# Kernel tuning notes

Hardware: AMD Instinct MI355X
Metric: run time of the kernel (lower is better)

## Reference

```python
import jax, jax.numpy as jnp
import numpy as np
import math

D_MODEL = 2048
N_HEADS = 16
D_HEAD = D_MODEL // N_HEADS
SCALE = 1.0 / math.sqrt(D_HEAD)


def setup_inputs() -> dict:
    key = jax.random.key(0)
    kx, kq, kk, kv, ko = jax.random.split(key, 5)
    x = jax.random.normal(kx, (2, 2048, D_MODEL), dtype=jnp.float32)
    W_q = jax.random.normal(kq, (D_MODEL, D_MODEL), dtype=jnp.float32)
    W_k = jax.random.normal(kk, (D_MODEL, D_MODEL), dtype=jnp.float32)
    W_v = jax.random.normal(kv, (D_MODEL, D_MODEL), dtype=jnp.float32) * math.sqrt(2.0 / D_MODEL)
    W_o = jax.random.normal(ko, (D_MODEL, D_MODEL), dtype=jnp.float32) * math.sqrt(2.0 / D_MODEL)
    return {"x": x, "W_q": W_q, "W_k": W_k, "W_v": W_v, "W_o": W_o}


def reference(x, W_q, W_k, W_v, W_o) -> jnp.ndarray:
    B, S, D = x.shape
    q = (x @ W_q).reshape(B, S, N_HEADS, D_HEAD)  # [b, q, h, dh]
    k = (x @ W_k).reshape(B, S, N_HEADS, D_HEAD)  # [b, k, h, dh]
    v = x @ W_v                                    # [b, k, d_model] (NOT split into heads)
    scores = jnp.einsum('bqhd,bkhd->bhqk', q, k)   # [b, h, q, k]
    # Faithful quirk: additive -1e9 causal mask applied BEFORE the scale.
    mask = jnp.triu(jnp.full((S, S), -1e9, dtype=scores.dtype), k=1)
    scores = (scores + mask) * SCALE
    probs = jax.nn.softmax(scores, axis=-1)
    # Faithful quirk: sums over heads h AND keys k against full-width v.
    out = jnp.einsum('bhqk,bkd->bqd', probs, v)    # [b, q, d_model]
    return out @ W_o
```

## Files before the change

kernel.cpp:

```cpp
#include <hip/hip_runtime.h>

typedef unsigned short u16;
typedef __attribute__((ext_vector_type(8))) short bf16x8;
typedef __attribute__((ext_vector_type(4))) float f32x4;

#define DEV __device__ __forceinline__
#define EXP2(x) __builtin_amdgcn_exp2f(x)
#define LOG2(x) __builtin_amdgcn_logf(x)

DEV u16 f2bf(float f) {
  union { float f; unsigned u; } v; v.f = f;
  unsigned r = v.u + 0x7fffu + ((v.u >> 16) & 1u);
  return (u16)(r >> 16);
}
DEV float bf2f(u16 h) {
  union { unsigned u; float f; } v; v.u = ((unsigned)h) << 16;
  return v.f;
}
DEV f32x4 mfma16(bf16x8 a, bf16x8 b, f32x4 c) {
  return __builtin_amdgcn_mfma_f32_16x16x32_bf16(a, b, c, 0, 0, 0);
}
DEV void cp16(const u16* g, u16* l) {
  __builtin_amdgcn_global_load_lds((__attribute__((address_space(1))) void*)g,
                                   (__attribute__((address_space(3))) void*)l, 16, 0, 0);
}

__global__ __launch_bounds__(256) void split_pair(const float4* __restrict__ x,
                                                  u16* __restrict__ hi, u16* __restrict__ lo) {
  const size_t i = (size_t)blockIdx.x * 256 + threadIdx.x;
  const float4 v = x[i];
  ushort4 h, l;
  h.x = f2bf(v.x); l.x = f2bf(v.x - bf2f(h.x));
  h.y = f2bf(v.y); l.y = f2bf(v.y - bf2f(h.y));
  h.z = f2bf(v.z); l.z = f2bf(v.z - bf2f(h.z));
  h.w = f2bf(v.w); l.w = f2bf(v.w - bf2f(h.w));
  *(ushort4*)&hi[i * 4] = h;
  *(ushort4*)&lo[i * 4] = l;
}

template<bool LO>
__global__ __launch_bounds__(256) void transpose_split(const float* __restrict__ W,
                                                       u16* __restrict__ Th, u16* __restrict__ Tl) {
  __shared__ float t[64][65];
  const int r0 = blockIdx.y * 64, c0 = blockIdx.x * 64;
  const int rr = threadIdx.x >> 4, c4 = (threadIdx.x & 15) * 4;
#pragma unroll
  for (int p = 0; p < 4; ++p) {
    const float4 v = *(const float4*)&W[(size_t)(r0 + p * 16 + rr) * 2048 + c0 + c4];
    t[p * 16 + rr][c4 + 0] = v.x; t[p * 16 + rr][c4 + 1] = v.y;
    t[p * 16 + rr][c4 + 2] = v.z; t[p * 16 + rr][c4 + 3] = v.w;
  }
  __syncthreads();
#pragma unroll
  for (int p = 0; p < 4; ++p) {
    const int cc = p * 16 + rr;
    const float v0 = t[c4 + 0][cc], v1 = t[c4 + 1][cc], v2 = t[c4 + 2][cc], v3 = t[c4 + 3][cc];
    ushort4 h;
    h.x = f2bf(v0); h.y = f2bf(v1); h.z = f2bf(v2); h.w = f2bf(v3);
    *(ushort4*)&Th[(size_t)(c0 + cc) * 2048 + r0 + c4] = h;
    if constexpr (LO) {
      ushort4 l;
      l.x = f2bf(v0 - bf2f(h.x)); l.y = f2bf(v1 - bf2f(h.y));
      l.z = f2bf(v2 - bf2f(h.z)); l.w = f2bf(v3 - bf2f(h.w));
      *(ushort4*)&Tl[(size_t)(c0 + cc) * 2048 + r0 + c4] = l;
    }
  }
}

template<bool SPLIT3, int OUTMODE, bool KLIM>
__global__ __launch_bounds__(256, 2) void gemm_bt(
    const u16* __restrict__ Aph, const u16* __restrict__ Apl,
    const u16* __restrict__ Bph, const u16* __restrict__ Bpl,
    const u16* __restrict__ Bph2, const u16* __restrict__ Bpl2,
    void* __restrict__ C0, void* __restrict__ C1,
    void* __restrict__ C0b, void* __restrict__ C1b,
    const int M, const int N, const int K, const int bShift) {
  extern __shared__ u16 lds[];
  constexpr int T_AL = 4096;
  constexpr int T_BH = SPLIT3 ? 8192 : 4096;
  constexpr int T_BL = 12288;
  if (blockIdx.z) { Bph = Bph2; Bpl = Bpl2; C0 = C0b; C1 = C1b; }
  const int tid = threadIdx.x;
  const int wave = tid >> 6, lane = tid & 63;
  const int li = lane & 15, l4 = lane >> 4;
  const int lin0 = ((int)blockIdx.y << 4) | (int)blockIdx.x;
  const int xcd = lin0 & 7, idx = lin0 >> 3;
  const int m0 = ((xcd << 2) | (idx & 3)) * 128;
  const int n0 = (idx >> 2) * 128;
  const int wr = (wave >> 1) * 64, wc = (wave & 1) * 64;
  const u16* Bh = Bph; const u16* Bl = Bpl;
  if (bShift) { const size_t s = (size_t)(m0 >> 11) * (size_t)bShift; Bh += s; if (SPLIT3) Bl += s; }

  const f32x4 fz = {0.f, 0.f, 0.f, 0.f};
  f32x4 acc[4][4];
#pragma unroll
  for (int m = 0; m < 4; ++m)
#pragma unroll
    for (int n = 0; n < 4; ++n) acc[m][n] = fz;

  const size_t aoff = (size_t)(m0 + (tid >> 2)) * K + (tid & 3) * 8;
  const size_t boff = (size_t)(n0 + (tid >> 2)) * K + (tid & 3) * 8;
  const size_t rstep = (size_t)64 * K;
  const int s0 = tid * 8, s1 = 2048 + tid * 8;
  const int abase = (wr + li) * 32 + l4 * 8;
  const int bbase = (wc + li) * 32 + l4 * 8;
  const int kEnd = KLIM ? ((m0 & 2047) + 128 < K ? (m0 & 2047) + 128 : K) : K;

#pragma unroll 1
  for (int k0 = 0; k0 < kEnd; k0 += 32) {
    cp16(Aph + aoff + k0,         &lds[s0]);
    cp16(Aph + aoff + rstep + k0, &lds[s1]);
    cp16(Bh + boff + k0,          &lds[T_BH + s0]);
    cp16(Bh + boff + rstep + k0,  &lds[T_BH + s1]);
    if constexpr (SPLIT3) {
      cp16(Apl + aoff + k0,         &lds[T_AL + s0]);
      cp16(Apl + aoff + rstep + k0, &lds[T_AL + s1]);
      cp16(Bl + boff + k0,          &lds[T_BL + s0]);
      cp16(Bl + boff + rstep + k0,  &lds[T_BL + s1]);
    }
    __syncthreads();
    bf16x8 af[4], bf_[4];
#pragma unroll
    for (int m = 0; m < 4; ++m) af[m] = *(const bf16x8*)&lds[abase + m * 512];
#pragma unroll
    for (int n = 0; n < 4; ++n) bf_[n] = *(const bf16x8*)&lds[T_BH + bbase + n * 512];
    if constexpr (SPLIT3) {
      bf16x8 alf[4], blf[4];
#pragma unroll
      for (int m = 0; m < 4; ++m) alf[m] = *(const bf16x8*)&lds[T_AL + abase + m * 512];
#pragma unroll
      for (int n = 0; n < 4; ++n) blf[n] = *(const bf16x8*)&lds[T_BL + bbase + n * 512];
#pragma unroll
      for (int m = 0; m < 4; ++m)
#pragma unroll
        for (int n = 0; n < 4; ++n) {
          acc[m][n] = mfma16(af[m], bf_[n], acc[m][n]);
          acc[m][n] = mfma16(af[m], blf[n], acc[m][n]);
          acc[m][n] = mfma16(alf[m], bf_[n], acc[m][n]);
        }
    } else {
#pragma unroll
      for (int m = 0; m < 4; ++m)
#pragma unroll
        for (int n = 0; n < 4; ++n)
          acc[m][n] = mfma16(af[m], bf_[n], acc[m][n]);
    }
    __syncthreads();
  }

#pragma unroll
  for (int m = 0; m < 4; ++m) {
#pragma unroll
    for (int n = 0; n < 4; ++n) {
      const int rg0 = m0 + wr + m * 16 + l4 * 4;
      const int cg  = n0 + wc + n * 16 + li;
      if constexpr (OUTMODE == 0) {
        u16* Ch = (u16*)C0; u16* Cl = (u16*)C1;
#pragma unroll
        for (int r = 0; r < 4; ++r) {
          const float v = acc[m][n][r];
          const u16 h = f2bf(v);
          Ch[(size_t)(rg0 + r) * N + cg] = h;
          Cl[(size_t)(rg0 + r) * N + cg] = f2bf(v - bf2f(h));
        }
      } else if constexpr (OUTMODE == 1) {
        u16* Cs = (u16*)C0;
#pragma unroll
        for (int r = 0; r < 4; ++r) Cs[(size_t)(rg0 + r) * N + cg] = f2bf(acc[m][n][r]);
      } else if constexpr (OUTMODE == 2) {
        u16* Vt = (u16*)C0;
        ushort4 pk;
        pk.x = f2bf(acc[m][n][0]); pk.y = f2bf(acc[m][n][1]);
        pk.z = f2bf(acc[m][n][2]); pk.w = f2bf(acc[m][n][3]);
        *(ushort4*)&Vt[(size_t)(rg0 >> 11) * 4194304 + (size_t)cg * 2048 + (rg0 & 2047)] = pk;
      } else {
        float* Cf = (float*)C0;
#pragma unroll
        for (int r = 0; r < 4; ++r) Cf[(size_t)(rg0 + r) * N + cg] = acc[m][n][r];
      }
    }
  }
}

#define C2EXP 0.1275174381027786f

__global__ __launch_bounds__(256) void attn_lse_part(
    const u16* __restrict__ Qh, const u16* __restrict__ Ql,
    const u16* __restrict__ Kh, const u16* __restrict__ Kl,
    float* __restrict__ Mp, float* __restrict__ Lp) {
  const int j = blockIdx.x, qt = 15 - (int)blockIdx.y, hb = blockIdx.z;
  const int b = hb >> 4, h = hb & 15;
  const int tid = threadIdx.x;
  const int nch = (qt >> 2) + 1;
  if (j >= nch) {
    if (tid < 128) {
      const size_t o = ((size_t)hb * 4 + j) * 2048 + qt * 128 + tid;
      Mp[o] = -3.0e38f; Lp[o] = 0.f;
    }
    return;
  }
  __shared__ __align__(16) u16 kb[16384];
  const int wave = tid >> 6, lane = tid & 63;
  const int li = lane & 15, l4 = lane >> 4;
  const int q0w = qt * 128 + wave * 32;
  const int rs = ((li << 6) | (l4 << 4)) ^ (((li >> 1) & 7) << 4);

  bf16x8 qfh[2][4], qfl[2][4];
#pragma unroll
  for (int mf = 0; mf < 2; ++mf) {
    const size_t qo = ((size_t)(b * 2048 + q0w + mf * 16 + li)) * 2048 + h * 128 + l4 * 8;
#pragma unroll
    for (int ks = 0; ks < 4; ++ks) {
      qfh[mf][ks] = *(const bf16x8*)&Qh[qo + ks * 32];
      qfl[mf][ks] = *(const bf16x8*)&Ql[qo + ks * 32];
    }
  }
  float m[2][4], l[2][4];
#pragma unroll
  for (int mf = 0; mf < 2; ++mf)
#pragma unroll
    for (int r = 0; r < 4; ++r) { m[mf][r] = -3.0e38f; l[mf][r] = 0.f; }

  const int kst = j * 8;
  const int ken = min(j * 8 + 8, qt * 2 + 2);
  const size_t kgbase = ((size_t)b * 2048) * 2048 + h * 128;
  const f32x4 fz = {0.f, 0.f, 0.f, 0.f};

#pragma unroll 1
  for (int t = kst; t < ken; ++t) {
    __syncthreads();
#pragma unroll
    for (int i = 0; i < 4; ++i) {
      const int o = (tid + i * 256) * 16;
      const int op = o ^ (((o >> 7) & 7) << 4);
      const int dck = op >> 12, s = (op >> 6) & 63, dl = (op >> 1) & 31;
      const size_t g = kgbase + (size_t)(t * 64 + s) * 2048 + dck * 32 + dl;
      cp16(Kh + g, kb + (o >> 1));
      cp16(Kl + g, kb + 8192 + (o >> 1));
    }
    __syncthreads();
#pragma unroll
    for (int sn = 0; sn < 4; ++sn) {
      if (64 * t + 16 * sn <= q0w + 31) {
        f32x4 a0 = fz, a1 = fz;
#pragma unroll
        for (int ks = 0; ks < 4; ++ks) {
          const bf16x8 kh = *(const bf16x8*)((const char*)kb + ks * 4096 + (sn << 10) + rs);
          const bf16x8 kl = *(const bf16x8*)((const char*)kb + 16384 + ks * 4096 + (sn << 10) + rs);
          a0 = mfma16(qfh[0][ks], kh, a0);
          a0 = mfma16(qfh[0][ks], kl, a0);
          a0 = mfma16(qfl[0][ks], kh, a0);
          a1 = mfma16(qfh[1][ks], kh, a1);
          a1 = mfma16(qfh[1][ks], kl, a1);
          a1 = mfma16(qfl[1][ks], kh, a1);
        }
        const int kg = t * 64 + sn * 16 + li;
#pragma unroll
        for (int r = 0; r < 4; ++r) {
          {
            const float aa = (kg <= q0w + l4 * 4 + r) ? a0[r] : -3.3e38f;
            if (__all(aa <= m[0][r])) {
              l[0][r] += EXP2((aa - m[0][r]) * C2EXP);
            } else {
              const float mn = fmaxf(m[0][r], aa);
              l[0][r] = l[0][r] * EXP2((m[0][r] - mn) * C2EXP) + EXP2((aa - mn) * C2EXP);
              m[0][r] = mn;
            }
          }
          {
            const float aa = (kg <= q0w + 16 + l4 * 4 + r) ? a1[r] : -3.3e38f;
            if (__all(aa <= m[1][r])) {
              l[1][r] += EXP2((aa - m[1][r]) * C2EXP);
            } else {
              const float mn = fmaxf(m[1][r], aa);
              l[1][r] = l[1][r] * EXP2((m[1][r] - mn) * C2EXP) + EXP2((aa - mn) * C2EXP);
              m[1][r] = mn;
            }
          }
        }
      }
    }
  }
#pragma unroll
  for (int off = 1; off <= 8; off <<= 1) {
#pragma unroll
    for (int mf = 0; mf < 2; ++mf)
#pragma unroll
      for (int r = 0; r < 4; ++r) {
        const float om = __shfl_xor(m[mf][r], off, 64);
        const float ol = __shfl_xor(l[mf][r], off, 64);
        const float mn = fmaxf(m[mf][r], om);
        l[mf][r] = l[mf][r] * EXP2((m[mf][r] - mn) * C2EXP) + ol * EXP2((om - mn) * C2EXP);
        m[mf][r] = mn;
      }
  }
  if (li == 0) {
#pragma unroll
    for (int mf = 0; mf < 2; ++mf)
#pragma unroll
      for (int r = 0; r < 4; ++r) {
        const size_t o = ((size_t)hb * 4 + j) * 2048 + q0w + mf * 16 + l4 * 4 + r;
        Mp[o] = m[mf][r];
        Lp[o] = l[mf][r];
      }
  }
}

__global__ __launch_bounds__(256) void attn_lse_merge(
    const float* __restrict__ Mp, const float* __restrict__ Lp, float* __restrict__ LSE) {
  const int id = blockIdx.x * 256 + threadIdx.x;
  const int q = id & 2047, hb = id >> 11;
  const size_t base = (size_t)hb * 4 * 2048 + q;
  float m = Mp[base], l = Lp[base];
#pragma unroll
  for (int jj = 1; jj < 4; ++jj) {
    const float om = Mp[base + jj * 2048];
    const float ol = Lp[base + jj * 2048];
    const float mn = fmaxf(m, om);
    l = l * EXP2((m - mn) * C2EXP) + ol * EXP2((om - mn) * C2EXP);
    m = mn;
  }
  LSE[(size_t)hb * 2048 + q] = m * C2EXP + LOG2(l);
}

__global__ __launch_bounds__(256) void attn_psum(
    const u16* __restrict__ Qh, const u16* __restrict__ Ql,
    const u16* __restrict__ Kh, const u16* __restrict__ Kl,
    const float* __restrict__ LSE, u16* __restrict__ Psum) {
  const int kt = blockIdx.x, qt = blockIdx.y, b = blockIdx.z;
  const int q0 = qt * 128, k0 = kt * 128;
  const int tid = threadIdx.x;

  if (kt > qt) {
    const size_t o = ((size_t)(b * 2048 + q0 + (tid >> 1))) * 2048 + k0 + (tid & 1) * 64;
    const uint4 z = {0u, 0u, 0u, 0u};
#pragma unroll
    for (int j2 = 0; j2 < 8; ++j2) *(uint4*)&Psum[o + j2 * 8] = z;
    return;
  }

  extern __shared__ u16 kb2[];
  const int wave = tid >> 6, lane = tid & 63;
  const int li = lane & 15, l4 = lane >> 4;
  const int q0w = q0 + wave * 32;
  const int rs = ((li << 6) | (l4 << 4)) ^ (((li >> 1) & 7) << 4);
  const int snmax = (kt == qt) ? (wave * 2 + 2) : 8;

  const f32x4 fz = {0.f, 0.f, 0.f, 0.f};
  f32x4 ps[2][8];
#pragma unroll
  for (int mf = 0; mf < 2; ++mf)
#pragma unroll
    for (int sn = 0; sn < 8; ++sn) ps[mf][sn] = fz;

  const size_t kgbase = ((size_t)(b * 2048 + k0)) * 2048;
  const size_t qbase0 = ((size_t)(b * 2048 + q0w + li)) * 2048 + l4 * 8;
  const size_t qbase1 = qbase0 + (size_t)16 * 2048;
  const size_t lbase  = (size_t)(b * 16) * 2048 + q0w + l4 * 4;

#pragma unroll 1
  for (int h = 0; h < 16; ++h) {
    __syncthreads();
#pragma unroll
    for (int i = 0; i < 8; ++i) {
      const int o = (tid + i * 256) * 16;
      const int op = o ^ (((o >> 7) & 7) << 4);
      const int dck = op >> 13, s = (op >> 6) & 127, dl = (op >> 1) & 31;
      const size_t g = kgbase + (size_t)s * 2048 + h * 128 + dck * 32 + dl;
      cp16(Kh + g, kb2 + (o >> 1));
      cp16(Kl + g, kb2 + 16384 + (o >> 1));
    }
    bf16x8 qfh0[4], qfl0[4], qfh1[4], qfl1[4];
    float clse[2][4];
#pragma unroll
    for (int ks = 0; ks < 4; ++ks) {
      qfh0[ks] = *(const bf16x8*)&Qh[qbase0 + (size_t)h * 128 + ks * 32];
      qfl0[ks] = *(const bf16x8*)&Ql[qbase0 + (size_t)h * 128 + ks * 32];
      qfh1[ks] = *(const bf16x8*)&Qh[qbase1 + (size_t)h * 128 + ks * 32];
      qfl1[ks] = *(const bf16x8*)&Ql[qbase1 + (size_t)h * 128 + ks * 32];
    }
#pragma unroll
    for (int mf = 0; mf < 2; ++mf)
#pragma unroll
      for (int r = 0; r < 4; ++r)
        clse[mf][r] = LSE[lbase + (size_t)h * 2048 + mf * 16 + r];
    __syncthreads();

#pragma unroll
    for (int sn = 0; sn < 8; ++sn) {
      if (sn < snmax) {
        f32x4 a0 = fz, a1 = fz;
#pragma unroll
        for (int ks = 0; ks < 4; ++ks) {
          const bf16x8 kh = *(const bf16x8*)((const char*)kb2 + ks * 8192 + (sn << 10) + rs);
          const bf16x8 kl = *(const bf16x8*)((const char*)kb2 + 32768 + ks * 8192 + (sn << 10) + rs);
          a0 = mfma16(qfh0[ks], kh, a0);
          a0 = mfma16(qfh0[ks], kl, a0);
          a0 = mfma16(qfl0[ks], kh, a0);
          a1 = mfma16(qfh1[ks], kh, a1);
          a1 = mfma16(qfh1[ks], kl, a1);
          a1 = mfma16(qfl1[ks], kh, a1);
        }
        const int kg = k0 + sn * 16 + li;
#pragma unroll
        for (int r = 0; r < 4; ++r) {
          if (kg <= q0w + l4 * 4 + r)      ps[0][sn][r] += EXP2(a0[r] * C2EXP - clse[0][r]);
          if (kg <= q0w + 16 + l4 * 4 + r) ps[1][sn][r] += EXP2(a1[r] * C2EXP - clse[1][r]);
        }
      }
    }
  }

#pragma unroll
  for (int mf = 0; mf < 2; ++mf)
#pragma unroll
    for (int sn = 0; sn < 8; ++sn) {
      const size_t o0 = ((size_t)(b * 2048 + q0w + mf * 16 + l4 * 4)) * 2048 + k0 + sn * 16 + li;
#pragma unroll
      for (int r = 0; r < 4; ++r) Psum[o0 + (size_t)r * 2048] = f2bf(ps[mf][sn][r]);
    }
}

extern "C" void kernel_launch(void* const* d_in, const int* in_sizes, int n_in,
                              void* d_out, int out_size, void* d_ws, size_t ws_size,
                              hipStream_t stream) {
  (void)in_sizes; (void)n_in; (void)out_size; (void)ws_size;
  const float* x  = (const float*)d_in[0];
  const float* Wq = (const float*)d_in[1];
  const float* Wk = (const float*)d_in[2];
  const float* Wv = (const float*)d_in[3];
  const float* Wo = (const float*)d_in[4];
  u16* ws = (u16*)d_ws;
  const size_t E8 = 8388608, E4 = 4194304;
  u16* xh = ws;
  u16* xl = ws + E8;
  u16* Qh = ws + 2 * E8;
  u16* Ql = ws + 3 * E8;
  u16* Kh = ws + 4 * E8;
  u16* Kl = ws + 5 * E8;
  u16* Vt = ws + 6 * E8;
  u16* WTh = ws + 7 * E8;
  u16* WTl = ws + 7 * E8 + E4;
  u16* WTb = ws + 7 * E8 + 2 * E4;
  u16* WkTh = Vt;
  u16* WkTl = Vt + E4;
  float* LSEf = (float*)WTl;
  float* Mp   = LSEf + 65536;
  float* Lp   = Mp + 262144;
  u16* Psum = xl;
  u16* out1 = xh;

  split_pair<<<8192, 256, 0, stream>>>((const float4*)x, xh, xl);

  dim3 tg(32, 32);

  transpose_split<true ><<<tg, 256, 0, stream>>>(Wq, WTh, WTl);
  transpose_split<true ><<<tg, 256, 0, stream>>>(Wk, WkTh, WkTl);
  transpose_split<false><<<tg, 256, 0, stream>>>(Wv, WTb, nullptr);

  gemm_bt<true, 0, false><<<dim3(16, 32, 2), 256, 32768, stream>>>(
      xh, xl, WTh, WTl, WkTh, WkTl, Qh, Ql, Kh, Kl, 4096, 2048, 2048, 0);

  gemm_bt<false, 2, false><<<dim3(16, 32), 256, 16384, stream>>>(
      xh, nullptr, WTb, nullptr, nullptr, nullptr, Vt, nullptr, nullptr, nullptr,
      4096, 2048, 2048, 0);

  attn_lse_part<<<dim3(4, 16, 32), 256, 0, stream>>>(Qh, Ql, Kh, Kl, Mp, Lp);
  attn_lse_merge<<<256, 256, 0, stream>>>(Mp, Lp, LSEf);
  attn_psum<<<dim3(16, 16, 2), 256, 65536, stream>>>(Qh, Ql, Kh, Kl, LSEf, Psum);

  gemm_bt<false, 1, true><<<dim3(16, 32), 256, 16384, stream>>>(
      Psum, nullptr, Vt, nullptr, nullptr, nullptr, out1, nullptr, nullptr, nullptr,
      4096, 2048, 2048, 4194304);

  transpose_split<false><<<tg, 256, 0, stream>>>(Wo, WTb, nullptr);
  gemm_bt<false, 3, false><<<dim3(16, 32), 256, 16384, stream>>>(
      out1, nullptr, WTb, nullptr, nullptr, nullptr, d_out, nullptr, nullptr, nullptr,
      4096, 2048, 2048, 0);
}
```

Before: 616.3 us.

## Fuse Q and K projections into one GEMM sharing A tiles; add MFMA priority hints

```diff
diff --git a/kernel.cpp b/kernel.cpp
--- a/kernel.cpp
+++ b/kernel.cpp
@@ -67,19 +67,13 @@
   }
 }
 
-template<bool SPLIT3, int OUTMODE, bool KLIM>
-__global__ __launch_bounds__(256, 2) void gemm_bt(
+__global__ __launch_bounds__(256, 2) void gemm_qk(
     const u16* __restrict__ Aph, const u16* __restrict__ Apl,
-    const u16* __restrict__ Bph, const u16* __restrict__ Bpl,
-    const u16* __restrict__ Bph2, const u16* __restrict__ Bpl2,
-    void* __restrict__ C0, void* __restrict__ C1,
-    void* __restrict__ C0b, void* __restrict__ C1b,
-    const int M, const int N, const int K, const int bShift) {
+    const u16* __restrict__ Bqh, const u16* __restrict__ Bql,
+    const u16* __restrict__ Bkh, const u16* __restrict__ Bkl,
+    u16* __restrict__ Qh, u16* __restrict__ Ql,
+    u16* __restrict__ Kh, u16* __restrict__ Kl) {
   extern __shared__ u16 lds[];
-  constexpr int T_AL = 4096;
-  constexpr int T_BH = SPLIT3 ? 8192 : 4096;
-  constexpr int T_BL = 12288;
-  if (blockIdx.z) { Bph = Bph2; Bpl = Bpl2; C0 = C0b; C1 = C1b; }
   const int tid = threadIdx.x;
   const int wave = tid >> 6, lane = tid & 63;
   const int li = lane & 15, l4 = lane >> 4;
@@ -88,8 +82,115 @@
   const int m0 = ((xcd << 2) | (idx & 3)) * 128;
   const int n0 = (idx >> 2) * 128;
   const int wr = (wave >> 1) * 64, wc = (wave & 1) * 64;
-  const u16* Bh = Bph; const u16* Bl = Bpl;
-  if (bShift) { const size_t s = (size_t)(m0 >> 11) * (size_t)bShift; Bh += s; if (SPLIT3) Bl += s; }
+
+  const f32x4 fz = {0.f, 0.f, 0.f, 0.f};
+  f32x4 accQ[4][4], accK[4][4];
+#pragma unroll
+  for (int m = 0; m < 4; ++m)
+#pragma unroll
+    for (int n = 0; n < 4; ++n) { accQ[m][n] = fz; accK[m][n] = fz; }
+
+  const size_t aoff = (size_t)(m0 + (tid >> 2)) * 2048 + (tid & 3) * 8;
+  const size_t boff = (size_t)(n0 + (tid >> 2)) * 2048 + (tid & 3) * 8;
+  const size_t rstep = (size_t)64 * 2048;
+  const int s0 = tid * 8, s1 = 2048 + tid * 8;
+  const int abase = (wr + li) * 32 + l4 * 8;
+  const int bbase = (wc + li) * 32 + l4 * 8;
+
+#pragma unroll 1
+  for (int k0 = 0; k0 < 2048; k0 += 32) {
+    cp16(Aph + aoff + k0,         &lds[s0]);
+    cp16(Aph + aoff + rstep + k0, &lds[s1]);
+    cp16(Apl + aoff + k0,         &lds[4096 + s0]);
+    cp16(Apl + aoff + rstep + k0, &lds[4096 + s1]);
+    cp16(Bqh + boff + k0,         &lds[8192 + s0]);
+    cp16(Bqh + boff + rstep + k0, &lds[8192 + s1]);
+    cp16(Bql + boff + k0,         &lds[12288 + s0]);
+    cp16(Bql + boff + rstep + k0, &lds[12288 + s1]);
+    cp16(Bkh + boff + k0,         &lds[16384 + s0]);
+    cp16(Bkh + boff + rstep + k0, &lds[16384 + s1]);
+    cp16(Bkl + boff + k0,         &lds[20480 + s0]);
+    cp16(Bkl + boff + rstep + k0, &lds[20480 + s1]);
+    __syncthreads();
+    bf16x8 af[4], alf[4];
+#pragma unroll
+    for (int m = 0; m < 4; ++m) {
+      af[m]  = *(const bf16x8*)&lds[abase + m * 512];
+      alf[m] = *(const bf16x8*)&lds[4096 + abase + m * 512];
+    }
+    {
+      bf16x8 bh[4], bl[4];
+#pragma unroll
+      for (int n = 0; n < 4; ++n) {
+        bh[n] = *(const bf16x8*)&lds[8192 + bbase + n * 512];
+        bl[n] = *(const bf16x8*)&lds[12288 + bbase + n * 512];
+      }
+#pragma unroll
+      for (int m = 0; m < 4; ++m)
+#pragma unroll
+        for (int n = 0; n < 4; ++n) {
+          accQ[m][n] = mfma16(af[m], bh[n], accQ[m][n]);
+          accQ[m][n] = mfma16(af[m], bl[n], accQ[m][n]);
+          accQ[m][n] = mfma16(alf[m], bh[n], accQ[m][n]);
+        }
+    }
+    {
+      bf16x8 bh[4], bl[4];
+#pragma unroll
+      for (int n = 0; n < 4; ++n) {
+        bh[n] = *(const bf16x8*)&lds[16384 + bbase + n * 512];
+        bl[n] = *(const bf16x8*)&lds[20480 + bbase + n * 512];
+      }
+#pragma unroll
+      for (int m = 0; m < 4; ++m)
+#pragma unroll
+        for (int n = 0; n < 4; ++n) {
+          accK[m][n] = mfma16(af[m], bh[n], accK[m][n]);
+          accK[m][n] = mfma16(af[m], bl[n], accK[m][n]);
+          accK[m][n] = mfma16(alf[m], bh[n], accK[m][n]);
+        }
+    }
+    __syncthreads();
+  }
+
+#pragma unroll
+  for (int m = 0; m < 4; ++m) {
+#pragma unroll
+    for (int n = 0; n < 4; ++n) {
+      const int rg0 = m0 + wr + m * 16 + l4 * 4;
+      const int cg  = n0 + wc + n * 16 + li;
+#pragma unroll
+      for (int r = 0; r < 4; ++r) {
+        const float vq = accQ[m][n][r];
+        const u16 hq = f2bf(vq);
+        Qh[(size_t)(rg0 + r) * 2048 + cg] = hq;
+        Ql[(size_t)(rg0 + r) * 2048 + cg] = f2bf(vq - bf2f(hq));
+        const float vk = accK[m][n][r];
+        const u16 hk = f2bf(vk);
+        Kh[(size_t)(rg0 + r) * 2048 + cg] = hk;
+        Kl[(size_t)(rg0 + r) * 2048 + cg] = f2bf(vk - bf2f(hk));
+      }
+    }
+  }
+}
+
+template<int OUTMODE, bool KLIM>
+__global__ __launch_bounds__(256, 2) void gemm_bt(
+    const u16* __restrict__ Aph, const u16* __restrict__ Bph,
+    void* __restrict__ C0,
+    const int M, const int N, const int K, const int bShift) {
+  extern __shared__ u16 lds[];
+  constexpr int T_BH = 4096;
+  const int tid = threadIdx.x;
+  const int wave = tid >> 6, lane = tid & 63;
+  const int li = lane & 15, l4 = lane >> 4;
+  const int lin0 = ((int)blockIdx.y << 4) | (int)blockIdx.x;
+  const int xcd = lin0 & 7, idx = lin0 >> 3;
+  const int m0 = ((xcd << 2) | (idx & 3)) * 128;
+  const int n0 = (idx >> 2) * 128;
+  const int wr = (wave >> 1) * 64, wc = (wave & 1) * 64;
+  const u16* Bh = Bph;
+  if (bShift) { const size_t s = (size_t)(m0 >> 11) * (size_t)bShift; Bh += s; }
 
   const f32x4 fz = {0.f, 0.f, 0.f, 0.f};
   f32x4 acc[4][4];
@@ -112,39 +213,17 @@
     cp16(Aph + aoff + rstep + k0, &lds[s1]);
     cp16(Bh + boff + k0,          &lds[T_BH + s0]);
     cp16(Bh + boff + rstep + k0,  &lds[T_BH + s1]);
-    if constexpr (SPLIT3) {
-      cp16(Apl + aoff + k0,         &lds[T_AL + s0]);
-      cp16(Apl + aoff + rstep + k0, &lds[T_AL + s1]);
-      cp16(Bl + boff + k0,          &lds[T_BL + s0]);
-      cp16(Bl + boff + rstep + k0,  &lds[T_BL + s1]);
-    }
     __syncthreads();
     bf16x8 af[4], bf_[4];
 #pragma unroll
     for (int m = 0; m < 4; ++m) af[m] = *(const bf16x8*)&lds[abase + m * 512];
 #pragma unroll
     for (int n = 0; n < 4; ++n) bf_[n] = *(const bf16x8*)&lds[T_BH + bbase + n * 512];
-    if constexpr (SPLIT3) {
-      bf16x8 alf[4], blf[4];
-#pragma unroll
-      for (int m = 0; m < 4; ++m) alf[m] = *(const bf16x8*)&lds[T_AL + abase + m * 512];
-#pragma unroll
-      for (int n = 0; n < 4; ++n) blf[n] = *(const bf16x8*)&lds[T_BL + bbase + n * 512];
-#pragma unroll
-      for (int m = 0; m < 4; ++m)
-#pragma unroll
-        for (int n = 0; n < 4; ++n) {
-          acc[m][n] = mfma16(af[m], bf_[n], acc[m][n]);
-          acc[m][n] = mfma16(af[m], blf[n], acc[m][n]);
-          acc[m][n] = mfma16(alf[m], bf_[n], acc[m][n]);
-        }
-    } else {
-#pragma unroll
-      for (int m = 0; m < 4; ++m)
-#pragma unroll
-        for (int n = 0; n < 4; ++n)
-          acc[m][n] = mfma16(af[m], bf_[n], acc[m][n]);
-    }
+#pragma unroll
+    for (int m = 0; m < 4; ++m)
+#pragma unroll
+      for (int n = 0; n < 4; ++n)
+        acc[m][n] = mfma16(af[m], bf_[n], acc[m][n]);
     __syncthreads();
   }
 
@@ -154,16 +233,7 @@
     for (int n = 0; n < 4; ++n) {
       const int rg0 = m0 + wr + m * 16 + l4 * 4;
       const int cg  = n0 + wc + n * 16 + li;
-      if constexpr (OUTMODE == 0) {
-        u16* Ch = (u16*)C0; u16* Cl = (u16*)C1;
-#pragma unroll
-        for (int r = 0; r < 4; ++r) {
-          const float v = acc[m][n][r];
-          const u16 h = f2bf(v);
-          Ch[(size_t)(rg0 + r) * N + cg] = h;
-          Cl[(size_t)(rg0 + r) * N + cg] = f2bf(v - bf2f(h));
-        }
-      } else if constexpr (OUTMODE == 1) {
+      if constexpr (OUTMODE == 1) {
         u16* Cs = (u16*)C0;
 #pragma unroll
         for (int r = 0; r < 4; ++r) Cs[(size_t)(rg0 + r) * N + cg] = f2bf(acc[m][n][r]);
@@ -243,6 +313,7 @@
     for (int sn = 0; sn < 4; ++sn) {
       if (64 * t + 16 * sn <= q0w + 31) {
         f32x4 a0 = fz, a1 = fz;
+        __builtin_amdgcn_s_setprio(1);
 #pragma unroll
         for (int ks = 0; ks < 4; ++ks) {
           const bf16x8 kh = *(const bf16x8*)((const char*)kb + ks * 4096 + (sn << 10) + rs);
@@ -254,6 +325,7 @@
           a1 = mfma16(qfh[1][ks], kl, a1);
           a1 = mfma16(qfl[1][ks], kh, a1);
         }
+        __builtin_amdgcn_s_setprio(0);
         const int kg = t * 64 + sn * 16 + li;
 #pragma unroll
         for (int r = 0; r < 4; ++r) {
@@ -390,6 +462,7 @@
     for (int sn = 0; sn < 8; ++sn) {
       if (sn < snmax) {
         f32x4 a0 = fz, a1 = fz;
+        __builtin_amdgcn_s_setprio(1);
 #pragma unroll
         for (int ks = 0; ks < 4; ++ks) {
           const bf16x8 kh = *(const bf16x8*)((const char*)kb2 + ks * 8192 + (sn << 10) + rs);
@@ -401,6 +474,7 @@
           a1 = mfma16(qfh1[ks], kl, a1);
           a1 = mfma16(qfl1[ks], kh, a1);
         }
+        __builtin_amdgcn_s_setprio(0);
         const int kg = k0 + sn * 16 + li;
 #pragma unroll
         for (int r = 0; r < 4; ++r) {
@@ -458,23 +532,20 @@
   transpose_split<true ><<<tg, 256, 0, stream>>>(Wk, WkTh, WkTl);
   transpose_split<false><<<tg, 256, 0, stream>>>(Wv, WTb, nullptr);
 
-  gemm_bt<true, 0, false><<<dim3(16, 32, 2), 256, 32768, stream>>>(
-      xh, xl, WTh, WTl, WkTh, WkTl, Qh, Ql, Kh, Kl, 4096, 2048, 2048, 0);
-
-  gemm_bt<false, 2, false><<<dim3(16, 32), 256, 16384, stream>>>(
-      xh, nullptr, WTb, nullptr, nullptr, nullptr, Vt, nullptr, nullptr, nullptr,
-      4096, 2048, 2048, 0);
+  gemm_qk<<<dim3(16, 32), 256, 49152, stream>>>(
+      xh, xl, WTh, WTl, WkTh, WkTl, Qh, Ql, Kh, Kl);
+
+  gemm_bt<2, false><<<dim3(16, 32), 256, 16384, stream>>>(
+      xh, WTb, Vt, 4096, 2048, 2048, 0);
 
   attn_lse_part<<<dim3(4, 16, 32), 256, 0, stream>>>(Qh, Ql, Kh, Kl, Mp, Lp);
   attn_lse_merge<<<256, 256, 0, stream>>>(Mp, Lp, LSEf);
   attn_psum<<<dim3(16, 16, 2), 256, 65536, stream>>>(Qh, Ql, Kh, Kl, LSEf, Psum);
 
-  gemm_bt<false, 1, true><<<dim3(16, 32), 256, 16384, stream>>>(
-      Psum, nullptr, Vt, nullptr, nullptr, nullptr, out1, nullptr, nullptr, nullptr,
-      4096, 2048, 2048, 4194304);
+  gemm_bt<1, true><<<dim3(16, 32), 256, 16384, stream>>>(
+      Psum, Vt, out1, 4096, 2048, 2048, 4194304);
 
   transpose_split<false><<<tg, 256, 0, stream>>>(Wo, WTb, nullptr);
-  gemm_bt<false, 3, false><<<dim3(16, 32), 256, 16384, stream>>>(
-      out1, nullptr, WTb, nullptr, nullptr, nullptr, d_out, nullptr, nullptr, nullptr,
-      4096, 2048, 2048, 0);
-}
+  gemm_bt<3, false><<<dim3(16, 32), 256, 16384, stream>>>(
+      out1, WTb, d_out, 4096, 2048, 2048, 0);
+}
```

Measured after the change: 565.8 us. 1.09x faster.
